# Kernel tuning notes

Hardware: AMD Instinct MI355X
Metric: run time of the kernel (lower is better)

Reference implementation:

```python
import jax, jax.numpy as jnp
import numpy as np

BS, N_STK, N_STK_PNT = 4, 32, 128
N_PNT = N_STK * N_STK_PNT
SP_IN, DN_IN = 128, 128
SP_OUT, DN_OUT = 256, 256
SP_NEAR, DN_NEAR = 2, 10
COOR = 128


def _conv2d(x, w, b, stride=(1, 1), pad='VALID'):
    # x [bs,C,H,W], w [O,I,kh,kw]
    y = jax.lax.conv_general_dilated(x, w, window_strides=stride, padding=pad,
                                     dimension_numbers=('NCHW', 'OIHW', 'NCHW'))
    return y + b[None, :, None, None]


def _fps(xyz, n_sample):
    # farthest point sampling. xyz [bs,n,c] -> [bs,n_sample] int32
    n = xyz.shape[1]

    def one(x):
        def body(i, state):
            idx, dist, far = state
            idx = idx.at[i].set(far)
            d = jnp.sum((x - x[far]) ** 2, axis=-1)
            dist = jnp.minimum(dist, d)
            return idx, dist, jnp.argmax(dist).astype(jnp.int32)

        idx0 = jnp.zeros((n_sample,), jnp.int32)
        dist0 = jnp.full((n,), 1e10, x.dtype)
        idx, _, _ = jax.lax.fori_loop(0, n_sample, body, (idx0, dist0, jnp.int32(0)))
        return idx

    return jax.vmap(one)(xyz)


def _gcn(x, W, b, g, bt, k):
    # DGCNN edge-conv. x [bs,c,n]; W [2c,co]
    xt = jnp.swapaxes(x, 1, 2)                                   # [bs,n,c]
    sq = jnp.sum(xt * xt, axis=-1)                               # [bs,n]
    dist = sq[:, :, None] - 2.0 * jnp.einsum('bnc,bmc->bnm', xt, xt) + sq[:, None, :]
    _, idx = jax.lax.top_k(-dist, k)                             # [bs,n,k]
    nbr = jax.vmap(lambda p, i: p[i])(xt, idx)                   # [bs,n,k,c]
    ctr = jnp.broadcast_to(xt[:, :, None, :], nbr.shape)
    edge = jnp.concatenate([ctr, nbr - ctr], axis=-1)            # [bs,n,k,2c]
    h = jnp.einsum('bnke,eo->bnko', edge, W) + b
    h = jax.nn.relu(g * h + bt)
    return jnp.swapaxes(jnp.max(h, axis=2), 1, 2)                # [bs,co,n]


def setup_inputs() -> dict:
    key = jax.random.key(0)
    ks = jax.random.split(key, 16)
    f32 = jnp.float32
    d = {
        'sparse_fea': jax.random.normal(ks[0], (BS, SP_IN, N_STK), f32),
        'dense_fea': jax.random.normal(ks[1], (BS, DN_IN, N_PNT), f32),
        'stk_coor': jax.random.normal(ks[2], (BS, N_STK, COOR), f32),
        # DenseToSparse: Conv2d(dn_in->dn_in, (1,3)) + BN
        'd2s_w': jax.random.normal(ks[3], (DN_IN, DN_IN, 1, 3), f32) * 0.05,
        'd2s_b': jnp.zeros((DN_IN,), f32),
        'd2s_g': jnp.ones((DN_IN,), f32),
        'd2s_bt': jnp.zeros((DN_IN,), f32),
        # sparse GCN: in = SP_IN + DN_IN, edge feat 2*in
        'sp_W': jax.random.normal(ks[4], (2 * (SP_IN + DN_IN), SP_OUT), f32) * 0.05,
        'sp_b': jnp.zeros((SP_OUT,), f32),
        'sp_g': jnp.ones((SP_OUT,), f32),
        'sp_bt': jnp.zeros((SP_OUT,), f32),
        # dense GCN: in = DN_IN + SP_IN
        'dn_W': jax.random.normal(ks[5], (2 * (DN_IN + SP_IN), DN_OUT), f32) * 0.05,
        'dn_b': jnp.zeros((DN_OUT,), f32),
        'dn_g': jnp.ones((DN_OUT,), f32),
        'dn_bt': jnp.zeros((DN_OUT,), f32),
        # DownSample: Conv2d(dn_out->dn_out, (1,3), stride (1,2), pad (0,1)) + BN
        'ds_w': jax.random.normal(ks[6], (DN_OUT, DN_OUT, 1, 3), f32) * 0.05,
        'ds_b': jnp.zeros((DN_OUT,), f32),
        'ds_g': jnp.ones((DN_OUT,), f32),
        'ds_bt': jnp.zeros((DN_OUT,), f32),
    }
    return d


def reference(sparse_fea, dense_fea, stk_coor,
              d2s_w, d2s_b, d2s_g, d2s_bt,
              sp_W, sp_b, sp_g, sp_bt,
              dn_W, dn_b, dn_g, dn_bt,
              ds_w, ds_b, ds_g, ds_bt):
    bs = sparse_fea.shape[0]
    df = dense_fea.reshape(bs, DN_IN, N_STK, N_STK_PNT)
    # DenseToSparse: conv (1,3) valid + BN(eval) + relu + max over stroke points
    h = _conv2d(df, d2s_w, d2s_b)
    h = jax.nn.relu(d2s_g[None, :, None, None] * h + d2s_bt[None, :, None, None])
    sp_from_dn = jnp.max(h, axis=3)                                    # [bs,dn_in,n_stk]
    union_sparse = jnp.concatenate([sparse_fea, sp_from_dn], axis=1)   # [bs,sp_in+dn_in,n_stk]
    # SparseToDense: broadcast stroke feature onto its points
    dn_from_sp = jnp.broadcast_to(sparse_fea[:, :, :, None], (bs, SP_IN, N_STK, N_STK_PNT))
    union_dense = jnp.concatenate([df, dn_from_sp], axis=1).reshape(bs, DN_IN + SP_IN, N_PNT)
    # GCN (DGCNN edge conv) updates
    sparse_up = _gcn(union_sparse, sp_W, sp_b, sp_g, sp_bt, SP_NEAR)   # [bs,SP_OUT,n_stk]
    dense_up = _gcn(union_dense, dn_W, dn_b, dn_g, dn_bt, DN_NEAR)     # [bs,DN_OUT,n_pnt]
    # DownSample: FPS on stroke coords, gather strokes, strided conv on points
    n_half = N_STK // 2
    fps_idx = _fps(stk_coor, n_half)                                   # [bs,n_half]
    stk_coor_s = jnp.take_along_axis(stk_coor, fps_idx[:, :, None], axis=1)
    sp_s = jnp.take_along_axis(jnp.swapaxes(sparse_up, 1, 2), fps_idx[:, :, None], axis=1)
    sp_s = jnp.swapaxes(sp_s, 1, 2)                                    # [bs,SP_OUT,n_half]
    dn = dense_up.reshape(bs, DN_OUT, N_STK, N_STK_PNT)
    dn = jnp.take_along_axis(dn, fps_idx[:, None, :, None], axis=2)    # [bs,DN_OUT,n_half,n_stk_pnt]
    dn = _conv2d(dn, ds_w, ds_b, stride=(1, 2), pad=[(0, 0), (1, 1)])
    dn = jax.nn.relu(ds_g[None, :, None, None] * dn + ds_bt[None, :, None, None])
    dn = dn.reshape(bs, DN_OUT, n_half * (N_STK_PNT // 2))
    return sp_s, dn, stk_coor_s
```

## Files before the change

### kernel.cpp

```cpp
#include <hip/hip_runtime.h>

#define NPNT 4096
#define NSTK 32

typedef _Float16 half8 __attribute__((ext_vector_type(8)));
typedef float f32x4 __attribute__((ext_vector_type(4)));
typedef unsigned long long u64;
typedef unsigned int u32;
typedef unsigned short u16;

static const size_t OFF_XT   = 0;
static const size_t OFF_P    = 4194304;
static const size_t OFF_Q    = 8388608;
static const size_t OFF_SQD  = 12582912;
static const size_t OFF_SPFD = 12599296;
static const size_t OFF_WSP  = 12746752;
static const size_t OFF_FPS  = 13566208;
static const size_t OFF_SD   = 13566272;

__device__ __forceinline__ void insertK(u64 lk[10], u64 k) {
  if (k >= lk[9]) return;
  lk[9] = k;
#pragma unroll
  for (int j = 9; j > 0; j--) {
    u64 a = lk[j-1], b2 = lk[j];
    bool sw = b2 < a;
    lk[j-1] = sw ? b2 : a;
    lk[j]   = sw ? a : b2;
  }
}

#define CASK(a, b) { u64 _x = (a), _y = (b); bool _s = _y < _x; \
  (a) = _s ? _y : _x; (b) = _s ? _x : _y; }

__device__ __forceinline__ void merge10(u64 lk[10], const u64 b[10]) {
  u64 c[10];
#pragma unroll
  for (int i = 0; i < 10; i++) { u64 t = b[9 - i]; u64 a = lk[i]; c[i] = a < t ? a : t; }
  CASK(c[0], c[5]); CASK(c[1], c[6]); CASK(c[2], c[7]); CASK(c[3], c[8]); CASK(c[4], c[9]);
  CASK(c[0], c[1]); CASK(c[1], c[2]); CASK(c[2], c[3]); CASK(c[3], c[4]);
  CASK(c[0], c[1]); CASK(c[1], c[2]); CASK(c[2], c[3]);
  CASK(c[0], c[1]); CASK(c[1], c[2]);
  CASK(c[0], c[1]);
  CASK(c[5], c[6]); CASK(c[6], c[7]); CASK(c[7], c[8]); CASK(c[8], c[9]);
  CASK(c[5], c[6]); CASK(c[6], c[7]); CASK(c[7], c[8]);
  CASK(c[5], c[6]); CASK(c[6], c[7]);
  CASK(c[5], c[6]);
#pragma unroll
  for (int i = 0; i < 10; i++) lk[i] = c[i];
}

__global__ __launch_bounds__(256) void k_pre(
    const float* __restrict__ df, const float* __restrict__ sf,
    const float* __restrict__ coor, const float* __restrict__ dnW,
    const float* __restrict__ d2sw, const float* __restrict__ d2scb,
    const float* __restrict__ d2sg, const float* __restrict__ d2sbt,
    const float* __restrict__ dsw,
    _Float16* __restrict__ XH, _Float16* __restrict__ XL, float* __restrict__ sqd,
    _Float16* __restrict__ WPh, _Float16* __restrict__ WPl,
    _Float16* __restrict__ WQh, _Float16* __restrict__ WQl,
    float* __restrict__ WDP, float* __restrict__ SD,
    float* __restrict__ spfd, int* __restrict__ fpsidx, float* __restrict__ out2) {
  __shared__ __align__(16) char SMEM[46080];
  const int bid = blockIdx.x;
  const int t = threadIdx.x;

  if (bid < 4) {
    int b = bid;
    float (*X)[132] = (float (*)[132])SMEM;
    float* dist = (float*)(SMEM + 16896);
    int* far_s  = (int*)(SMEM + 17024);
    int* sel    = (int*)(SMEM + 17028);
    for (int idx = t; idx < 32 * 32; idx += 256) {
      int r = idx >> 5, q = idx & 31;
      *(float4*)&X[r][q * 4] = *(const float4*)&coor[((size_t)b * 32 + r) * 128 + q * 4];
    }
    if (t < 32) dist[t] = 1e10f;
    if (t == 0) *far_s = 0;
    __syncthreads();
    for (int it = 0; it < 16; it++) {
      int far = *far_s;
      if (t == 0) sel[it] = far;
      if (t < 32) {
        float d = 0.0f;
        for (int c = 0; c < 128; c++) { float dd = X[t][c] - X[far][c]; d = fmaf(dd, dd, d); }
        float dm = dist[t];
        dist[t] = d < dm ? d : dm;
      }
      __syncthreads();
      if (t == 0) {
        float best = -1.0f; int bi = 0;
        for (int m = 0; m < 32; m++) if (dist[m] > best) { best = dist[m]; bi = m; }
        *far_s = bi;
      }
      __syncthreads();
    }
    if (t < 16) fpsidx[b * 16 + t] = sel[t];
    __syncthreads();
    for (int idx = t; idx < 16 * 32; idx += 256) {
      int j = idx >> 5, q = idx & 31;
      *(float4*)&out2[((size_t)b * 16 + j) * 128 + q * 4] = *(const float4*)&X[sel[j]][q * 4];
    }
  } else if (bid < 8) {
    int b = bid - 4;
    float* Xs = (float*)SMEM;
    for (int k = t; k < 1024; k += 256)
      *(float4*)&Xs[k * 4] = *(const float4*)&sf[(size_t)b * 4096 + k * 4];
    __syncthreads();
#pragma unroll
    for (int rep = 0; rep < 4; rep++) {
      int p = t + rep * 256;
      int s = p >> 5, u = p & 31;
      float acc = 0.0f;
      for (int c = 0; c < 128; c++) {
        float d = Xs[c * 32 + s] - Xs[c * 32 + u];
        acc = fmaf(d, d, acc);
      }
      SD[(size_t)b * 1024 + p] = acc;
    }
  } else if (bid < 264) {
    int idx0 = bid - 8;
    int b = idx0 & 3, n0 = (idx0 >> 2) * 64;
    int s0 = n0 >> 7;
    float (*T)[68] = (float (*)[68])SMEM;
    _Float16* Sh = (_Float16*)(SMEM + 34816);
    _Float16* Sl = (_Float16*)(SMEM + 35072);
    {
      int c = t >> 1, nh = (t & 1) * 32;
      const float* src = &df[((size_t)b * 128 + c) * NPNT + n0 + nh];
#pragma unroll
      for (int j = 0; j < 8; j++) *(float4*)&T[c][nh + j * 4] = *(const float4*)&src[j * 4];
    }
    if (t < 128) {
      float x = sf[((size_t)b * 128 + t) * NSTK + s0];
      _Float16 hi = (_Float16)x;
      Sh[t] = hi; Sl[t] = (_Float16)(x - (float)hi);
    }
    __syncthreads();
    {
      int n = t >> 2, cseg = (t & 3) * 32;
      size_t base = ((size_t)b * NPNT + n0 + n) * 256;
      float s = 0.0f;
#pragma unroll
      for (int k = 0; k < 4; k++) {
        half8 hv, lv, shv, slv;
#pragma unroll
        for (int e = 0; e < 8; e++) {
          float x = T[cseg + k * 8 + e][n];
          s = fmaf(x, x, s);
          _Float16 hi = (_Float16)x;
          hv[e] = hi; lv[e] = (_Float16)(x - (float)hi);
          shv[e] = Sh[cseg + k * 8 + e];
          slv[e] = Sl[cseg + k * 8 + e];
        }
        *(half8*)&XH[base + cseg + k * 8] = hv;
        *(half8*)&XL[base + cseg + k * 8] = lv;
        *(half8*)&XH[base + 128 + cseg + k * 8] = shv;
        *(half8*)&XL[base + 128 + cseg + k * 8] = slv;
      }
      s += __shfl_xor(s, 1);
      s += __shfl_xor(s, 2);
      if ((t & 3) == 0) sqd[(size_t)b * NPNT + n0 + n] = s;
    }
  } else if (bid < 520) {
    int idx0 = bid - 264;
    int b = idx0 & 3, o0 = ((idx0 >> 2) & 1) * 64, s = idx0 >> 3;
    int n0 = s * 128;
    float (*A)[64]   = (float (*)[64])SMEM;
    float (*Bs)[132] = (float (*)[132])(SMEM + 24576);
    float (*Dr)[17]  = (float (*)[17])(SMEM + 41472);
    float acc[4][8];
#pragma unroll
    for (int i = 0; i < 4; i++)
#pragma unroll
      for (int j = 0; j < 8; j++) acc[i][j] = 0.0f;
    int tn = t & 15, to = t >> 4;
    for (int ic = 0; ic < 128; ic += 32) {
      {
        int ol = t >> 2, q = t & 3;
        const float* src = &d2sw[((size_t)(o0 + ol) * 128 + ic) * 3 + q * 24];
#pragma unroll
        for (int r = 0; r < 6; r++) {
          float4 v = *(const float4*)&src[r * 4];
          int e = q * 24 + r * 4;
          A[e+0][ol] = v.x; A[e+1][ol] = v.y; A[e+2][ol] = v.z; A[e+3][ol] = v.w;
        }
      }
      for (int idx = t; idx < 32 * 33; idx += 256) {
        int row = idx / 33, f4 = idx % 33;
        int nb = n0 + f4 * 4;
        const float* srow = &df[((size_t)b * 128 + ic + row) * NPNT];
        float4 v;
        if (nb + 3 < NPNT) v = *(const float4*)&srow[nb];
        else {
          v.x = srow[nb   < NPNT ? nb   : NPNT-1];
          v.y = srow[nb+1 < NPNT ? nb+1 : NPNT-1];
          v.z = srow[nb+2 < NPNT ? nb+2 : NPNT-1];
          v.w = srow[nb+3 < NPNT ? nb+3 : NPNT-1];
        }
        *(float4*)&Bs[row][f4 * 4] = v;
      }
      __syncthreads();
#pragma unroll 2
      for (int ii = 0; ii < 32; ii++) {
        float bv[12];
        *(float4*)&bv[0] = *(const float4*)&Bs[ii][tn * 8];
        *(float4*)&bv[4] = *(const float4*)&Bs[ii][tn * 8 + 4];
        *(float4*)&bv[8] = *(const float4*)&Bs[ii][tn * 8 + 8];
#pragma unroll
        for (int kw = 0; kw < 3; kw++) {
          float4 av = *(const float4*)&A[ii * 3 + kw][to * 4];
#pragma unroll
          for (int j = 0; j < 8; j++) {
            float bvj = bv[kw + j];
            acc[0][j] = fmaf(av.x, bvj, acc[0][j]);
            acc[1][j] = fmaf(av.y, bvj, acc[1][j]);
            acc[2][j] = fmaf(av.z, bvj, acc[2][j]);
            acc[3][j] = fmaf(av.w, bvj, acc[3][j]);
          }
        }
      }
      __syncthreads();
    }
#pragma unroll
    for (int i = 0; i < 4; i++) {
      int o = o0 + to * 4 + i;
      float gg = d2sg[o], bb = d2scb[o], bo = d2sbt[o];
      float m = 0.0f;
#pragma unroll
      for (int j = 0; j < 8; j++) {
        int p = tn * 8 + j;
        if (p < 126) {
          float v = fmaf(gg, acc[i][j] + bb, bo);
          v = v > 0.0f ? v : 0.0f;
          m = v > m ? v : m;
        }
      }
      Dr[to * 4 + i][tn] = m;
    }
    __syncthreads();
    if (t < 64) {
      float m = 0.0f;
#pragma unroll
      for (int k = 0; k < 16; k++) m = Dr[t][k] > m ? Dr[t][k] : m;
      spfd[((size_t)b * 128 + o0 + t) * NSTK + s] = m;
    }
  } else if (bid < 776) {
    int k = bid - 520, o = t;
    float w1 = dnW[(size_t)k * 256 + o];
    float w2 = dnW[(size_t)(k + 256) * 256 + o];
    float p = w1 - w2;
    _Float16 ph = (_Float16)p;  WPh[(size_t)o * 256 + k] = ph;
    WPl[(size_t)o * 256 + k] = (_Float16)(p - (float)ph);
    _Float16 qh = (_Float16)w2; WQh[(size_t)o * 256 + k] = qh;
    WQl[(size_t)o * 256 + k] = (_Float16)(w2 - (float)qh);
  } else {
    int o = bid - 776;
    const float* src = &dsw[(size_t)o * 768];
    float* dst = &WDP[(size_t)o * 768];
#pragma unroll
    for (int kw = 0; kw < 3; kw++)
      dst[kw * 256 + t] = src[t * 3 + kw];
  }
}

__global__ __launch_bounds__(256) void k_sparse_mono(const float* __restrict__ sf,
    const float* __restrict__ spfd, const int* __restrict__ fps, const float* __restrict__ W,
    const float* __restrict__ g, const float* __restrict__ cb, const float* __restrict__ bt,
    float* __restrict__ out0) {
  int b = blockIdx.x, t = threadIdx.x;
  __shared__ float X[32][260];
  __shared__ float Qs[32][256];
  __shared__ float D[32][33];
  __shared__ float sq[32];
  __shared__ int idxs_s[64];
  __shared__ int fps_s[16];
  for (int idx = t; idx < 32 * 256; idx += 256) {
    int n = idx >> 8, c = idx & 255;
    float v = (c < 128) ? sf[((size_t)b * 128 + c) * NSTK + n]
                        : spfd[((size_t)b * 128 + (c - 128)) * NSTK + n];
    X[n][c] = v;
  }
  if (t < 16) fps_s[t] = fps[b * 16 + t];
  __syncthreads();
  if (t < 32) {
    float s = 0.0f;
    for (int c = 0; c < 256; c++) s = fmaf(X[t][c], X[t][c], s);
    sq[t] = s;
  }
  __syncthreads();
  {
    int n = t >> 3;
    for (int mg = 0; mg < 4; mg++) {
      int m = (t & 7) + mg * 8;
      float dot = 0.0f;
      for (int c = 0; c < 256; c++) dot = fmaf(X[n][c], X[m][c], dot);
      D[n][m] = (sq[n] - 2.0f * dot) + sq[m];
    }
  }
  __syncthreads();
  if (t < 32) {
    float d0 = 1e30f, d1 = 1e30f; int i0 = 0, i1 = 0;
    for (int m = 0; m < 32; m++) {
      float d = D[t][m];
      if (d < d0) { d1 = d0; i1 = i0; d0 = d; i0 = m; }
      else if (d < d1) { d1 = d; i1 = m; }
    }
    idxs_s[t * 2 + 0] = i0;
    idxs_s[t * 2 + 1] = i1;
  }
  const int o = t;
#pragma unroll 1
  for (int nc = 0; nc < 4; nc++) {
    float acc[8];
#pragma unroll
    for (int nn = 0; nn < 8; nn++) acc[nn] = 0.0f;
    for (int c4 = 0; c4 < 64; c4++) {
      float4 xv[8];
#pragma unroll
      for (int nn = 0; nn < 8; nn++) xv[nn] = *(const float4*)&X[nc * 8 + nn][c4 * 4];
      int c = c4 * 4;
      float w0 = W[(size_t)(c + 256) * 256 + o];
      float w1 = W[(size_t)(c + 257) * 256 + o];
      float w2 = W[(size_t)(c + 258) * 256 + o];
      float w3 = W[(size_t)(c + 259) * 256 + o];
#pragma unroll
      for (int nn = 0; nn < 8; nn++) {
        acc[nn] = fmaf(xv[nn].x, w0, acc[nn]);
        acc[nn] = fmaf(xv[nn].y, w1, acc[nn]);
        acc[nn] = fmaf(xv[nn].z, w2, acc[nn]);
        acc[nn] = fmaf(xv[nn].w, w3, acc[nn]);
      }
    }
#pragma unroll
    for (int nn = 0; nn < 8; nn++) Qs[nc * 8 + nn][o] = acc[nn];
  }
  float pacc[16];
#pragma unroll 1
  for (int jc = 0; jc < 2; jc++) {
    int fs[8];
#pragma unroll
    for (int jj = 0; jj < 8; jj++) fs[jj] = fps_s[jc * 8 + jj];
    float acc[8];
#pragma unroll
    for (int jj = 0; jj < 8; jj++) acc[jj] = 0.0f;
    for (int c4 = 0; c4 < 64; c4++) {
      float4 xv[8];
#pragma unroll
      for (int jj = 0; jj < 8; jj++) xv[jj] = *(const float4*)&X[fs[jj]][c4 * 4];
      int c = c4 * 4;
      float p0 = W[(size_t)(c + 0) * 256 + o] - W[(size_t)(c + 256) * 256 + o];
      float p1 = W[(size_t)(c + 1) * 256 + o] - W[(size_t)(c + 257) * 256 + o];
      float p2 = W[(size_t)(c + 2) * 256 + o] - W[(size_t)(c + 258) * 256 + o];
      float p3 = W[(size_t)(c + 3) * 256 + o] - W[(size_t)(c + 259) * 256 + o];
#pragma unroll
      for (int jj = 0; jj < 8; jj++) {
        acc[jj] = fmaf(xv[jj].x, p0, acc[jj]);
        acc[jj] = fmaf(xv[jj].y, p1, acc[jj]);
        acc[jj] = fmaf(xv[jj].z, p2, acc[jj]);
        acc[jj] = fmaf(xv[jj].w, p3, acc[jj]);
      }
    }
#pragma unroll
    for (int jj = 0; jj < 8; jj++) pacc[jc * 8 + jj] = acc[jj];
  }
  __syncthreads();
  float gg = g[o], bb = cb[o], bo = bt[o];
#pragma unroll
  for (int j = 0; j < 16; j++) {
    int n = fps_s[j];
    int i0 = idxs_s[n * 2 + 0], i1 = idxs_s[n * 2 + 1];
    float p = pacc[j];
    float h0 = fmaf(gg, p + Qs[i0][o] + bb, bo); h0 = h0 > 0.0f ? h0 : 0.0f;
    float h1 = fmaf(gg, p + Qs[i1][o] + bb, bo); h1 = h1 > 0.0f ? h1 : 0.0f;
    out0[((size_t)b * 256 + o) * 16 + j] = h0 > h1 ? h0 : h1;
  }
}

#define STAGE(ch2_, p_) { \
  int srow = t >> 2, scol = (t & 3) * 16; \
  size_t gp = (bofs + (size_t)(m0 + (ch2_) * 64 + srow)) * 256 + (p_) * 64 + scol; \
  float4 gh0 = *(const float4*)&XH[gp]; float4 gh1 = *(const float4*)&XH[gp + 8]; \
  float4 gl0 = *(const float4*)&XL[gp]; float4 gl1 = *(const float4*)&XL[gp + 8]; \
  int lo = srow * 72 + scol; \
  *(float4*)&BshH[lo] = gh0; *(float4*)&BshH[lo + 8] = gh1; \
  *(float4*)&BshL[lo] = gl0; *(float4*)&BshL[lo + 8] = gl1; }

#define DWU(wv_, r_, c_) DwU[(((wv_) * 16 + (r_)) * 68) + (c_)]

__global__ __launch_bounds__(256, 4) void k_knn_mfma(const _Float16* __restrict__ XH,
    const _Float16* __restrict__ XL, const float* __restrict__ sqd, const float* __restrict__ SD,
    const int* __restrict__ fps, u32* __restrict__ pkd, u16* __restrict__ pki) {
  const int h = blockIdx.x, rb = blockIdx.y, b = blockIdx.z;
  const int t = threadIdx.x;
  const int w = t >> 6, L = t & 63;
  const int c15 = L & 15, q = L >> 4;
  const int jst = rb >> 1;
  const int ph = (rb & 1) * 64;
  const int s_stk = fps[b * 16 + jst];
  const int nsrc = s_stk * 128 + ph + w * 16;
  const int rc0 = rb * 64 + w * 16;
  const size_t bofs = (size_t)b * NPNT;

  __shared__ __align__(16) char SMEM[18432];
  _Float16* const BshH = (_Float16*)SMEM;
  _Float16* const BshL = (_Float16*)(SMEM + 64 * 72 * 2);
  unsigned* const DwU = (unsigned*)SMEM;

  half8 ah[4], al[4];
  {
    const _Float16* ap  = XH + (bofs + nsrc + c15) * 256 + q * 8;
    const _Float16* apl = XL + (bofs + nsrc + c15) * 256 + q * 8;
#pragma unroll
    for (int ch = 0; ch < 4; ch++) {
      ah[ch] = *(const half8*)(ap + ch * 32);
      al[ch] = *(const half8*)(apl + ch * 32);
    }
  }
  float snr[4];
#pragma unroll
  for (int r = 0; r < 4; r++) snr[r] = sqd[bofs + nsrc + q * 4 + r];

  u64 lk[10];
#pragma unroll
  for (int j = 0; j < 10; j++) lk[j] = ~0ull;

  const bool own_here = ((s_stk >> 1) == h);
  const int r_sel = L >> 2, sl = L & 3;
  const int u0 = own_here ? s_stk : (h * 2);
  const int u1 = own_here ? (s_stk ^ 1) : (h * 2 + 1);

#pragma unroll 1
  for (int it = 0; it < 2; it++) {
    const int u = (it == 0) ? u0 : u1;
    const int m0 = u * 128;
    const float SDv = SD[((size_t)b * 32 + s_stk) * 32 + u];

#pragma unroll 1
    for (int ch2 = 0; ch2 < 2; ch2++) {
      float smv[4];
#pragma unroll
      for (int cg = 0; cg < 4; cg++) smv[cg] = sqd[bofs + m0 + ch2 * 64 + cg * 16 + c15];

      f32x4 zz = {0.0f, 0.0f, 0.0f, 0.0f};
      f32x4 acc[4];
#pragma unroll
      for (int cg = 0; cg < 4; cg++) acc[cg] = zz;

      __syncthreads();
      STAGE(ch2, 0);
      __syncthreads();
#pragma unroll
      for (int chl = 0; chl < 2; chl++) {
#pragma unroll
        for (int cg = 0; cg < 4; cg++) {
          int lo = (cg * 16 + c15) * 72 + chl * 32 + q * 8;
          half8 bh = *(const half8*)&BshH[lo];
          half8 bl = *(const half8*)&BshL[lo];
          acc[cg] = __builtin_amdgcn_mfma_f32_16x16x32_f16(ah[chl], bh, acc[cg], 0, 0, 0);
          acc[cg] = __builtin_amdgcn_mfma_f32_16x16x32_f16(ah[chl], bl, acc[cg], 0, 0, 0);
          acc[cg] = __builtin_amdgcn_mfma_f32_16x16x32_f16(al[chl], bh, acc[cg], 0, 0, 0);
        }
      }
      __syncthreads();
      STAGE(ch2, 1);
      __syncthreads();
#pragma unroll
      for (int chl = 0; chl < 2; chl++) {
#pragma unroll
        for (int cg = 0; cg < 4; cg++) {
          int lo = (cg * 16 + c15) * 72 + chl * 32 + q * 8;
          half8 bh = *(const half8*)&BshH[lo];
          half8 bl = *(const half8*)&BshL[lo];
          acc[cg] = __builtin_amdgcn_mfma_f32_16x16x32_f16(ah[2 + chl], bh, acc[cg], 0, 0, 0);
          acc[cg] = __builtin_amdgcn_mfma_f32_16x16x32_f16(ah[2 + chl], bl, acc[cg], 0, 0, 0);
          acc[cg] = __builtin_amdgcn_mfma_f32_16x16x32_f16(al[2 + chl], bh, acc[cg], 0, 0, 0);
        }
      }
      __syncthreads();

#pragma unroll
      for (int cg = 0; cg < 4; cg++) {
        float basec = SDv + smv[cg];
#pragma unroll
        for (int r = 0; r < 4; r++) {
          float d = fmaf(-2.0f, acc[cg][r], snr[r] + basec);
          unsigned uu = __float_as_uint(d);
          unsigned kk = uu ^ ((unsigned)((int)uu >> 31) | 0x80000000u);
          DWU(w, q * 4 + r, cg * 16 + c15) = kk;
        }
      }
#pragma unroll
      for (int jj = 0; jj < 4; jj++) {
        uint4 kv = *(const uint4*)&DWU(w, r_sel, jj * 16 + sl * 4);
        int ib = m0 + ch2 * 64 + jj * 16 + sl * 4;
        insertK(lk, ((u64)kv.x << 32) | (unsigned)(ib + 0));
        insertK(lk, ((u64)kv.y << 32) | (unsigned)(ib + 1));
        insertK(lk, ((u64)kv.z << 32) | (unsigned)(ib + 2));
        insertK(lk, ((u64)kv.w << 32) | (unsigned)(ib + 3));
      }
    }
  }

#pragma unroll
  for (int m = 1; m <= 2; m <<= 1) {
    u64 o[10];
#pragma unroll
    for (int j = 0; j < 10; j++) o[j] = __shfl_xor(lk[j], m);
    merge10(lk, o);
  }
  if (sl == 0) {
    size_t row = (size_t)b * 2048 + rc0 + r_sel;
    u32* dk = &pkd[(row * 16 + h) * 10];
    u16* di = &pki[(row * 16 + h) * 10];
#pragma unroll
    for (int j = 0; j < 10; j++) {
      dk[j] = (u32)(lk[j] >> 32);
      di[j] = (u16)(lk[j] & 0xffffull);
    }
  }
}

__global__ __launch_bounds__(256) void k_build_M(const float* __restrict__ Pc, const float* __restrict__ Qp,
    const u32* __restrict__ pkd, const u16* __restrict__ pki, float* __restrict__ M) {
  int pc = blockIdx.x, j = blockIdx.y, b = blockIdx.z;
  int t = threadIdx.x;
  __shared__ int knn_s[16][10];
  {
    int rr = t >> 4, ll = t & 15;
    size_t row = (size_t)b * 2048 + j * 128 + pc * 16 + rr;
    const u32* kd = &pkd[(row * 16 + ll) * 10];
    const u16* ki = &pki[(row * 16 + ll) * 10];
    u64 lk[10];
#pragma unroll
    for (int jj = 0; jj < 10; jj++) lk[jj] = ((u64)kd[jj] << 32) | (u64)ki[jj];
#pragma unroll
    for (int m = 1; m <= 8; m <<= 1) {
      u64 o[10];
#pragma unroll
      for (int jj = 0; jj < 10; jj++) o[jj] = __shfl_xor(lk[jj], m);
      merge10(lk, o);
    }
    if (ll == 0) {
#pragma unroll
      for (int jj = 0; jj < 10; jj++) knn_s[rr][jj] = (int)(lk[jj] & 0xffffull);
    }
  }
  __syncthreads();
#pragma unroll 1
  for (int pi = 0; pi < 16; pi++) {
    size_t m = ((size_t)b * 16 + j) * 128 + pc * 16 + pi;
    float pv = Pc[m * 256 + t];
    float mx = 0.0f;
#pragma unroll
    for (int k = 0; k < 10; k++) {
      float qv = Qp[((size_t)b * NPNT + knn_s[pi][k]) * 256 + t];
      float h = pv + qv;
      mx = h > mx ? h : mx;
    }
    M[m * 256 + t] = mx;
  }
}

__global__ __launch_bounds__(256, 2) void k_pq_mfma(const _Float16* __restrict__ XH, const _Float16* __restrict__ XL,
    const _Float16* __restrict__ WPh, const _Float16* __restrict__ WPl,
    const _Float16* __restrict__ WQh, const _Float16* __restrict__ WQl,
    const int* __restrict__ fps, const float* __restrict__ g, const float* __restrict__ cb,
    const float* __restrict__ bt, float* __restrict__ Pc, float* __restrict__ Qp) {
  const int b = blockIdx.z;
  const int t = threadIdx.x, w = t >> 6, L = t & 63;
  const int c15 = L & 15, q = L >> 4;
  const int ow = blockIdx.y * 128 + (w >> 1) * 64;
  const size_t bofs = (size_t)b * NPNT;
  f32x4 zz = {0.0f, 0.0f, 0.0f, 0.0f};

  {
    const int nw = blockIdx.x * 32 + (w & 1) * 16;
    f32x4 accQ[4];
#pragma unroll
    for (int cg = 0; cg < 4; cg++) accQ[cg] = zz;
    const _Float16* ap  = XH + (bofs + nw + c15) * 256 + q * 8;
    const _Float16* apl = XL + (bofs + nw + c15) * 256 + q * 8;
#pragma unroll
    for (int ch = 0; ch < 8; ch++) {
      half8 a_h = *(const half8*)(ap + ch * 32);
      half8 a_l = *(const half8*)(apl + ch * 32);
#pragma unroll
      for (int cg = 0; cg < 4; cg++) {
        size_t wb = (size_t)(ow + cg * 16 + c15) * 256 + ch * 32 + q * 8;
        half8 bqh = *(const half8*)(WQh + wb);
        half8 bql = *(const half8*)(WQl + wb);
        accQ[cg] = __builtin_amdgcn_mfma_f32_16x16x32_f16(a_h, bqh, accQ[cg], 0, 0, 0);
        accQ[cg] = __builtin_amdgcn_mfma_f32_16x16x32_f16(a_h, bql, accQ[cg], 0, 0, 0);
        accQ[cg] = __builtin_amdgcn_mfma_f32_16x16x32_f16(a_l, bqh, accQ[cg], 0, 0, 0);
      }
    }
#pragma unroll
    for (int cg = 0; cg < 4; cg++) {
      int o = ow + cg * 16 + c15;
      float gg = g[o];
#pragma unroll
      for (int r = 0; r < 4; r++) {
        Qp[(bofs + nw + q * 4 + r) * 256 + o] = gg * accQ[cg][r];
      }
    }
  }

  if (blockIdx.x < 64) {
    const int m0 = blockIdx.x * 32 + (w & 1) * 16;
    const int jst = m0 >> 7;
    const int pbase = m0 & 127;
    const int nsrc = fps[b * 16 + jst] * 128 + pbase;
    f32x4 accP[4];
#pragma unroll
    for (int cg = 0; cg < 4; cg++) accP[cg] = zz;
    const _Float16* ap  = XH + (bofs + nsrc + c15) * 256 + q * 8;
    const _Float16* apl = XL + (bofs + nsrc + c15) * 256 + q * 8;
#pragma unroll
    for (int ch = 0; ch < 8; ch++) {
      half8 a_h = *(const half8*)(ap + ch * 32);
      half8 a_l = *(const half8*)(apl + ch * 32);
#pragma unroll
      for (int cg = 0; cg < 4; cg++) {
        size_t wb = (size_t)(ow + cg * 16 + c15) * 256 + ch * 32 + q * 8;
        half8 bph = *(const half8*)(WPh + wb);
        half8 bpl = *(const half8*)(WPl + wb);
        accP[cg] = __builtin_amdgcn_mfma_f32_16x16x32_f16(a_h, bph, accP[cg], 0, 0, 0);
        accP[cg] = __builtin_amdgcn_mfma_f32_16x16x32_f16(a_h, bpl, accP[cg], 0, 0, 0);
        accP[cg] = __builtin_amdgcn_mfma_f32_16x16x32_f16(a_l, bph, accP[cg], 0, 0, 0);
      }
    }
#pragma unroll
    for (int cg = 0; cg < 4; cg++) {
      int o = ow + cg * 16 + c15;
      float gg = g[o], bb = cb[o], bo = bt[o];
#pragma unroll
      for (int r = 0; r < 4; r++) {
        Pc[(((size_t)b * 16 + jst) * 128 + pbase + q * 4 + r) * 256 + o] =
            fmaf(gg, accP[cg][r] + bb, bo);
      }
    }
  }
}

__global__ __launch_bounds__(256) void k_ds_gemm(const float* __restrict__ WDP, const float* __restrict__ M,
    const float* __restrict__ cb, const float* __restrict__ g, const float* __restrict__ bt,
    float* __restrict__ out1) {
  int j = blockIdx.x, o0 = blockIdx.y * 64, b = blockIdx.z;
  int j0 = j * 64;
  int t = threadIdx.x;
  __shared__ float A[32][68];
  __shared__ float Bs[32][68];
  float acc[4][4];
#pragma unroll
  for (int i = 0; i < 4; i++)
#pragma unroll
    for (int jj = 0; jj < 4; jj++) acc[i][jj] = 0.0f;
  int tj = t & 15, to = t >> 4;
  for (int kc = 0; kc < 768; kc += 32) {
    {
      int ol = t >> 2, q = t & 3;
      const float* src = &WDP[(size_t)(o0 + ol) * 768 + kc + q * 8];
      float4 v0 = *(const float4*)src, v1 = *(const float4*)(src + 4);
      int cc = q * 8;
      A[cc+0][ol] = v0.x; A[cc+1][ol] = v0.y; A[cc+2][ol] = v0.z; A[cc+3][ol] = v0.w;
      A[cc+4][ol] = v1.x; A[cc+5][ol] = v1.y; A[cc+6][ol] = v1.z; A[cc+7][ol] = v1.w;
    }
    {
      int jl = t >> 2, q = t & 3;
      int kw = kc >> 8, cbl = (kc & 255) + q * 8;
      int p = 2 * jl - 1 + kw;
      float4 v0, v1;
      if (p >= 0) {
        const float* src = &M[(((size_t)b * 16 + j) * 128 + p) * 256 + cbl];
        v0 = *(const float4*)src; v1 = *(const float4*)(src + 4);
      } else {
        v0.x = v0.y = v0.z = v0.w = 0.0f; v1 = v0;
      }
      int cc = q * 8;
      Bs[cc+0][jl] = v0.x; Bs[cc+1][jl] = v0.y; Bs[cc+2][jl] = v0.z; Bs[cc+3][jl] = v0.w;
      Bs[cc+4][jl] = v1.x; Bs[cc+5][jl] = v1.y; Bs[cc+6][jl] = v1.z; Bs[cc+7][jl] = v1.w;
    }
    __syncthreads();
#pragma unroll 4
    for (int k = 0; k < 32; k++) {
      float4 a = *(const float4*)&A[k][to * 4];
      float4 bv = *(const float4*)&Bs[k][tj * 4];
      float av[4] = {a.x, a.y, a.z, a.w};
      float bb[4] = {bv.x, bv.y, bv.z, bv.w};
#pragma unroll
      for (int i = 0; i < 4; i++)
#pragma unroll
        for (int jj = 0; jj < 4; jj++)
          acc[i][jj] = fmaf(av[i], bb[jj], acc[i][jj]);
    }
    __syncthreads();
  }
#pragma unroll
  for (int i = 0; i < 4; i++) {
    int o = o0 + to * 4 + i;
    float gg = g[o], bb = cb[o], bo = bt[o];
    float4 v;
    float x0 = fmaf(gg, acc[i][0] + bb, bo); v.x = x0 > 0.0f ? x0 : 0.0f;
    float x1 = fmaf(gg, acc[i][1] + bb, bo); v.y = x1 > 0.0f ? x1 : 0.0f;
    float x2 = fmaf(gg, acc[i][2] + bb, bo); v.z = x2 > 0.0f ? x2 : 0.0f;
    float x3 = fmaf(gg, acc[i][3] + bb, bo); v.w = x3 > 0.0f ? x3 : 0.0f;
    *(float4*)&out1[((size_t)b * 256 + o) * 1024 + j0 + tj * 4] = v;
  }
}

extern "C" void kernel_launch(void* const* d_in, const int* in_sizes, int n_in,
                              void* d_out, int out_size, void* d_ws, size_t ws_size,
                              hipStream_t stream) {
  (void)in_sizes; (void)n_in; (void)out_size; (void)ws_size;
  const float* sf    = (const float*)d_in[0];
  const float* df    = (const float*)d_in[1];
  const float* coor  = (const float*)d_in[2];
  const float* d2sw  = (const float*)d_in[3];
  const float* d2sb  = (const float*)d_in[4];
  const float* d2sg  = (const float*)d_in[5];
  const float* d2sbt = (const float*)d_in[6];
  const float* spW   = (const float*)d_in[7];
  const float* spb   = (const float*)d_in[8];
  const float* spg   = (const float*)d_in[9];
  const float* spbt  = (const float*)d_in[10];
  const float* dnW   = (const float*)d_in[11];
  const float* dnb   = (const float*)d_in[12];
  const float* dng   = (const float*)d_in[13];
  const float* dnbt  = (const float*)d_in[14];
  const float* dsw   = (const float*)d_in[15];
  const float* dsb   = (const float*)d_in[16];
  const float* dsg   = (const float*)d_in[17];
  const float* dsbt  = (const float*)d_in[18];

  float* ws   = (float*)d_ws;
  float* Pc   = ws + OFF_P;
  float* Qp   = ws + OFF_Q;
  float* SQD  = ws + OFF_SQD;
  float* SPFD = ws + OFF_SPFD;
  int*   FPS  = (int*)(ws + OFF_FPS);
  float* SD   = ws + OFF_SD;
  _Float16* XT2H = (_Float16*)(ws + OFF_XT);
  _Float16* XT2L = XT2H + (size_t)4 * NPNT * 256;
  float* Mb = ws + OFF_XT;
  _Float16* WPh = (_Float16*)(ws + OFF_WSP);
  _Float16* WPl = WPh + 65536;
  _Float16* WQh = WPh + 131072;
  _Float16* WQl = WPh + 196608;
  float* WDP = ws + OFF_WSP + 131072;
  u32* PKD = (u32*)(ws + OFF_P + 2097152);
  u16* PKI = (u16*)(ws + OFF_P + 2097152 + 1310720);

  float* out0 = (float*)d_out;
  float* out1 = out0 + 16384;
  float* out2 = out1 + 1048576;

  k_pre<<<dim3(1032), 256, 0, stream>>>(df, sf, coor, dnW, d2sw, d2sb, d2sg, d2sbt, dsw,
                                        XT2H, XT2L, SQD, WPh, WPl, WQh, WQl, WDP, SD,
                                        SPFD, FPS, out2);
  k_sparse_mono<<<dim3(4), 256, 0, stream>>>(sf, SPFD, FPS, spW, spg, spb, spbt, out0);
  k_pq_mfma<<<dim3(128, 2, 4), 256, 0, stream>>>(XT2H, XT2L, WPh, WPl, WQh, WQl,
                                                 FPS, dng, dnb, dnbt, Pc, Qp);
  k_knn_mfma<<<dim3(16, 32, 4), 256, 0, stream>>>(XT2H, XT2L, SQD, SD, FPS, PKD, PKI);
  k_build_M<<<dim3(8, 16, 4), 256, 0, stream>>>(Pc, Qp, PKD, PKI, Mb);
  k_ds_gemm<<<dim3(16, 4, 4), 256, 0, stream>>>(WDP, Mb, dsb, dsg, dsbt, out1);
}
```

Baseline: 455.1 us.

## Split sparse GCN kernel across output-channel groups to use more blocks

```diff
diff --git a/kernel.cpp b/kernel.cpp
--- a/kernel.cpp
+++ b/kernel.cpp
@@ -264,22 +264,23 @@
   }
 }
 
-__global__ __launch_bounds__(256) void k_sparse_mono(const float* __restrict__ sf,
+__global__ __launch_bounds__(256) void k_sparse_mono2(const float* __restrict__ sf,
     const float* __restrict__ spfd, const int* __restrict__ fps, const float* __restrict__ W,
     const float* __restrict__ g, const float* __restrict__ cb, const float* __restrict__ bt,
     float* __restrict__ out0) {
-  int b = blockIdx.x, t = threadIdx.x;
+  int b = blockIdx.x, og = blockIdx.y;
+  int t = threadIdx.x;
   __shared__ float X[32][260];
-  __shared__ float Qs[32][256];
+  __shared__ float Qs[32][33];
+  __shared__ float Pl[16][33];
+  __shared__ float sq[32];
   __shared__ float D[32][33];
-  __shared__ float sq[32];
   __shared__ int idxs_s[64];
   __shared__ int fps_s[16];
   for (int idx = t; idx < 32 * 256; idx += 256) {
     int n = idx >> 8, c = idx & 255;
-    float v = (c < 128) ? sf[((size_t)b * 128 + c) * NSTK + n]
+    X[n][c] = (c < 128) ? sf[((size_t)b * 128 + c) * NSTK + n]
                         : spfd[((size_t)b * 128 + (c - 128)) * NSTK + n];
-    X[n][c] = v;
   }
   if (t < 16) fps_s[t] = fps[b * 16 + t];
   __syncthreads();
@@ -309,71 +310,64 @@
     idxs_s[t * 2 + 0] = i0;
     idxs_s[t * 2 + 1] = i1;
   }
-  const int o = t;
-#pragma unroll 1
-  for (int nc = 0; nc < 4; nc++) {
-    float acc[8];
-#pragma unroll
-    for (int nn = 0; nn < 8; nn++) acc[nn] = 0.0f;
+  const int ol = t & 31, sg = t >> 5;
+  const int o = og * 32 + ol;
+  {
+    float acc[4] = {0.0f, 0.0f, 0.0f, 0.0f};
     for (int c4 = 0; c4 < 64; c4++) {
-      float4 xv[8];
-#pragma unroll
-      for (int nn = 0; nn < 8; nn++) xv[nn] = *(const float4*)&X[nc * 8 + nn][c4 * 4];
       int c = c4 * 4;
       float w0 = W[(size_t)(c + 256) * 256 + o];
       float w1 = W[(size_t)(c + 257) * 256 + o];
       float w2 = W[(size_t)(c + 258) * 256 + o];
       float w3 = W[(size_t)(c + 259) * 256 + o];
 #pragma unroll
-      for (int nn = 0; nn < 8; nn++) {
-        acc[nn] = fmaf(xv[nn].x, w0, acc[nn]);
-        acc[nn] = fmaf(xv[nn].y, w1, acc[nn]);
-        acc[nn] = fmaf(xv[nn].z, w2, acc[nn]);
-        acc[nn] = fmaf(xv[nn].w, w3, acc[nn]);
-      }
-    }
-#pragma unroll
-    for (int nn = 0; nn < 8; nn++) Qs[nc * 8 + nn][o] = acc[nn];
-  }
-  float pacc[16];
-#pragma unroll 1
-  for (int jc = 0; jc < 2; jc++) {
-    int fs[8];
-#pragma unroll
-    for (int jj = 0; jj < 8; jj++) fs[jj] = fps_s[jc * 8 + jj];
-    float acc[8];
-#pragma unroll
-    for (int jj = 0; jj < 8; jj++) acc[jj] = 0.0f;
+      for (int k = 0; k < 4; k++) {
+        float4 xv = *(const float4*)&X[sg * 4 + k][c];
+        acc[k] = fmaf(xv.x, w0, acc[k]);
+        acc[k] = fmaf(xv.y, w1, acc[k]);
+        acc[k] = fmaf(xv.z, w2, acc[k]);
+        acc[k] = fmaf(xv.w, w3, acc[k]);
+      }
+    }
+#pragma unroll
+    for (int k = 0; k < 4; k++) Qs[sg * 4 + k][ol] = acc[k];
+  }
+  if (sg < 4) {
+    int fs[4];
+#pragma unroll
+    for (int k = 0; k < 4; k++) fs[k] = fps_s[sg * 4 + k];
+    float acc[4] = {0.0f, 0.0f, 0.0f, 0.0f};
     for (int c4 = 0; c4 < 64; c4++) {
-      float4 xv[8];
-#pragma unroll
-      for (int jj = 0; jj < 8; jj++) xv[jj] = *(const float4*)&X[fs[jj]][c4 * 4];
       int c = c4 * 4;
       float p0 = W[(size_t)(c + 0) * 256 + o] - W[(size_t)(c + 256) * 256 + o];
       float p1 = W[(size_t)(c + 1) * 256 + o] - W[(size_t)(c + 257) * 256 + o];
       float p2 = W[(size_t)(c + 2) * 256 + o] - W[(size_t)(c + 258) * 256 + o];
       float p3 = W[(size_t)(c + 3) * 256 + o] - W[(size_t)(c + 259) * 256 + o];
 #pragma unroll
-      for (int jj = 0; jj < 8; jj++) {
-        acc[jj] = fmaf(xv[jj].x, p0, acc[jj]);
-        acc[jj] = fmaf(xv[jj].y, p1, acc[jj]);
-        acc[jj] = fmaf(xv[jj].z, p2, acc[jj]);
-        acc[jj] = fmaf(xv[jj].w, p3, acc[jj]);
-      }
-    }
-#pragma unroll
-    for (int jj = 0; jj < 8; jj++) pacc[jc * 8 + jj] = acc[jj];
+      for (int k = 0; k < 4; k++) {
+        float4 xv = *(const float4*)&X[fs[k]][c];
+        acc[k] = fmaf(xv.x, p0, acc[k]);
+        acc[k] = fmaf(xv.y, p1, acc[k]);
+        acc[k] = fmaf(xv.z, p2, acc[k]);
+        acc[k] = fmaf(xv.w, p3, acc[k]);
+      }
+    }
+#pragma unroll
+    for (int k = 0; k < 4; k++) Pl[sg * 4 + k][ol] = acc[k];
   }
   __syncthreads();
-  float gg = g[o], bb = cb[o], bo = bt[o];
-#pragma unroll
-  for (int j = 0; j < 16; j++) {
-    int n = fps_s[j];
-    int i0 = idxs_s[n * 2 + 0], i1 = idxs_s[n * 2 + 1];
-    float p = pacc[j];
-    float h0 = fmaf(gg, p + Qs[i0][o] + bb, bo); h0 = h0 > 0.0f ? h0 : 0.0f;
-    float h1 = fmaf(gg, p + Qs[i1][o] + bb, bo); h1 = h1 > 0.0f ? h1 : 0.0f;
-    out0[((size_t)b * 256 + o) * 16 + j] = h0 > h1 ? h0 : h1;
+  if (t < 32) {
+    int oo = og * 32 + t;
+    float gg = g[oo], bb = cb[oo], bo = bt[oo];
+#pragma unroll
+    for (int j = 0; j < 16; j++) {
+      int n = fps_s[j];
+      int i0 = idxs_s[n * 2 + 0], i1 = idxs_s[n * 2 + 1];
+      float p = Pl[j][t];
+      float h0 = fmaf(gg, p + Qs[i0][t] + bb, bo); h0 = h0 > 0.0f ? h0 : 0.0f;
+      float h1 = fmaf(gg, p + Qs[i1][t] + bb, bo); h1 = h1 > 0.0f ? h1 : 0.0f;
+      out0[((size_t)b * 256 + oo) * 16 + j] = h0 > h1 ? h0 : h1;
+    }
   }
 }
 
@@ -758,7 +752,7 @@
   k_pre<<<dim3(1032), 256, 0, stream>>>(df, sf, coor, dnW, d2sw, d2sb, d2sg, d2sbt, dsw,
                                         XT2H, XT2L, SQD, WPh, WPl, WQh, WQl, WDP, SD,
                                         SPFD, FPS, out2);
-  k_sparse_mono<<<dim3(4), 256, 0, stream>>>(sf, SPFD, FPS, spW, spg, spb, spbt, out0);
+  k_sparse_mono2<<<dim3(4, 8), 256, 0, stream>>>(sf, SPFD, FPS, spW, spg, spb, spbt, out0);
   k_pq_mfma<<<dim3(128, 2, 4), 256, 0, stream>>>(XT2H, XT2L, WPh, WPl, WQh, WQl,
                                                  FPS, dng, dnb, dnbt, Pc, Qp);
   k_knn_mfma<<<dim3(16, 32, 4), 256, 0, stream>>>(XT2H, XT2L, SQD, SD, FPS, PKD, PKI);
```

Result: faster. 409.7 us, median of 2 (-10.0%).
